# Kernel optimization log

Measured on AMD Instinct MI355X. Metric: run time of the kernel, lower is better.

## Reference

```python
import jax, jax.numpy as jnp
import numpy as np

# -------- configuration (production-scale segmentation head) --------
BS, C, H, W = 8, 256, 96, 96
N = H * W          # nodes in the spanning tree (flattened pixels)
E = N - 1          # spanning-tree edge count
ZETA_G = 0.01      # default zeta_g of Global_APro.forward


def setup_inputs() -> dict:
    key = jax.random.key(0)
    k1, k2 = jax.random.split(key)
    feature_in = jax.random.normal(k1, (BS, 1, H, W), dtype=jnp.float32)
    # scaled so norm2 distances over C=256 channels stay O(1..10)
    embed_in = 0.1 * jax.random.normal(k2, (BS, C, H, W), dtype=jnp.float32)
    # Random spanning trees, one per batch element. Edges are topologically
    # ordered: edge e connects parent=src[e] < child=tgt[e]=e+1, so processing
    # edges in order is a valid root->leaf sweep (and reversed is leaf->root).
    rng = np.random.default_rng(0)
    trees = []
    children = np.arange(1, N, dtype=np.int32)
    for _ in range(BS):
        parents = np.floor(rng.random(E) * np.arange(1, N)).astype(np.int32)
        trees.append(np.stack([parents, children], axis=1))
    tree = jnp.asarray(np.stack(trees, axis=0))  # [BS, E, 2] int32
    return {"feature_in": feature_in, "embed_in": embed_in, "tree": tree}


def _gp_single(f, wgt, src, tgt):
    """Global affinity propagation (tree filter) on one tree.
    Computes out_i = sum_j A_ij f_j / sum_j A_ij with A_ij = prod of edge
    affinities along the unique tree path i->j, via the classic two-pass DP.
    f: [N], wgt/src/tgt: [E] (edges topologically ordered, parent=src).
    """
    ones = jnp.ones_like(f)

    def up(carry, xs):                 # leaf -> root aggregation
        S, Z = carry
        s, t, we = xs
        S = S.at[s].add(we * S[t])
        Z = Z.at[s].add(we * Z[t])
        return (S, Z), None

    (S, Z), _ = jax.lax.scan(up, (f, ones), (src, tgt, wgt), reverse=True)

    def down(carry, xs):               # root -> leaf propagation
        F, G = carry
        s, t, we = xs
        F = F.at[t].set(we * F[s] + (1.0 - we * we) * F[t])
        G = G.at[t].set(we * G[s] + (1.0 - we * we) * G[t])
        return (F, G), None

    (F, G), _ = jax.lax.scan(down, (S, Z), (src, tgt, wgt))
    return F / G


def reference(feature_in, embed_in, tree):
    bs, c, h, w = embed_in.shape
    n = h * w
    emb = embed_in.reshape(bs, c, n)               # [bs, c, N]
    src = tree[:, :, 0]                            # [bs, E]
    tgt = tree[:, :, 1]                            # [bs, E]
    # gather node embeddings along tree edges (get_true_index)
    gather = jax.vmap(lambda e, i: e[:, i])        # [c, N], [E] -> [c, E]
    src_node = gather(emb, src)                    # [bs, c, E]
    tgt_node = gather(emb, tgt)                    # [bs, c, E]
    diff = src_node - tgt_node
    dist = jnp.sum(diff * diff, axis=1)            # norm2_distance -> [bs, E]
    wgt = jnp.exp(-ZETA_G * dist)                  # edge affinity
    f = feature_in.reshape(bs, n)                  # [bs, N]
    out = jax.vmap(_gp_single)(f, wgt, src, tgt)   # [bs, N]
    return out.reshape(bs, 1, h, w)
```

## Files before the change

### kernel.cpp

```cpp
#include <hip/hip_runtime.h>
#include <hip/hip_bf16.h>
#include <hip/hip_fp16.h>

#define BS 8
#define C  256
#define N  9216
#define E  9215
#define MAXD 128
#define LVL_STRIDE 192
#define NARROW 64
#define CPG 8
#define NG  (C / CPG)

typedef __attribute__((address_space(1))) const void GVoid;
typedef __attribute__((address_space(3))) void LVoid;

__global__ __launch_bounds__(1024) void setup_kernel(const float* __restrict__ emb,
                                                     const int* __restrict__ tree,
                                                     float* __restrict__ distG,
                                                     int* __restrict__ uparr,
                                                     int* __restrict__ lvlOff) {
    __shared__ int P[N];
    __shared__ int U[N];
    __shared__ int cnt8[MAXD * 8];
    __shared__ int tot[MAXD];
    __shared__ int sc1[MAXD];
    __shared__ int off[MAXD + 1];
    __shared__ int maxd_sh;
    const int tid = threadIdx.x;

    if (blockIdx.x >= BS) {
        const int wb = blockIdx.x - BS;
        const int b  = wb & 7;
        const int c0 = (wb >> 3) * CPG;
        const int wave = tid >> 6, lane = tid & 63;

        float* cur = (float*)P;
        float* nxt = (float*)U;

        int se[9];
        #pragma unroll
        for (int k = 0; k < 9; ++k) {
            int e = tid + k * 1024;
            se[k] = (e < E) ? tree[((size_t)b * E + e) * 2] : 0;
        }
        float acc[9];
        #pragma unroll
        for (int k = 0; k < 9; ++k) acc[k] = 0.f;

        const float* rowbase = emb + ((size_t)b * C + c0) * N;
        {
            const float* src = rowbase;
            for (int chk = wave; chk < 36; chk += 16)
                __builtin_amdgcn_global_load_lds(
                    (GVoid*)(src + chk * 256 + lane * 4),
                    (LVoid*)(cur + chk * 256), 16, 0, 0);
        }
        __syncthreads();

        for (int cc = 0; cc < CPG; ++cc) {
            if (cc + 1 < CPG) {
                const float* src = rowbase + (size_t)(cc + 1) * N;
                for (int chk = wave; chk < 36; chk += 16)
                    __builtin_amdgcn_global_load_lds(
                        (GVoid*)(src + chk * 256 + lane * 4),
                        (LVoid*)(nxt + chk * 256), 16, 0, 0);
            }
            #pragma unroll
            for (int k = 0; k < 9; ++k) {
                int e = tid + k * 1024;
                if (e < E) {
                    float d = cur[se[k]] - cur[e + 1];
                    acc[k] += d * d;
                }
            }
            __syncthreads();
            float* t = cur; cur = nxt; nxt = t;
        }
        #pragma unroll
        for (int k = 0; k < 9; ++k) {
            int e = tid + k * 1024;
            if (e < E) atomicAdd(&distG[(size_t)b * N + e], acc[k]);
        }
        return;
    }

    const int b = blockIdx.x;
    const int* tb = tree + b * E * 2;

    for (int t = tid; t < N; t += 1024)
        P[t] = (t == 0) ? 0 : (tb[(t - 1) * 2] | (1 << 16));
    for (int i = tid; i < MAXD * 8; i += 1024) cnt8[i] = 0;
    if (tid == 0) maxd_sh = 1;
    __syncthreads();

    for (int r = 0; r < 3; ++r) {
        for (int t = tid; t < N; t += 1024) {
            int p = P[t];
            int a = p & 0xffff;
            if (a == 0) U[t] = p;
            else {
                int pa = P[a];
                U[t] = (pa & 0xffff) | (((p >> 16) + (pa >> 16)) << 16);
            }
        }
        __syncthreads();
        for (int t = tid; t < N; t += 1024) {
            int p = U[t];
            int a = p & 0xffff;
            if (a == 0) P[t] = p;
            else {
                int pa = U[a];
                P[t] = (pa & 0xffff) | (((p >> 16) + (pa >> 16)) << 16);
            }
        }
        __syncthreads();
    }

    for (int t = 1 + tid; t < N; t += 1024) {
        int d = P[t] >> 16;
        atomicAdd(&cnt8[d * 8 + (tid >> 7)], 1);
    }
    __syncthreads();

    for (int d = tid; d < MAXD; d += 1024) {
        int s = 0;
        #pragma unroll
        for (int k = 0; k < 8; ++k) {
            int v = cnt8[d * 8 + k];
            cnt8[d * 8 + k] = s;
            s += v;
        }
        tot[d] = s;
        if (s > 0) atomicMax(&maxd_sh, d);
    }
    __syncthreads();

    {
        int* src = tot; int* dst = sc1;
        for (int step = 1; step < MAXD; step <<= 1) {
            for (int d = tid; d < MAXD; d += 1024)
                dst[d] = src[d] + ((d >= step) ? src[d - step] : 0);
            __syncthreads();
            int* tmp = src; src = dst; dst = tmp;
        }
        for (int d = tid; d < MAXD; d += 1024) off[d + 1] = src[d];
        if (tid == 0) off[0] = 0;
    }
    __syncthreads();

    if (tid == 0) {
        int md = maxd_sh;
        int lo = 0;
        while (lo < md && off[lo + 2] - off[lo + 1] <= NARROW) ++lo;
        int hi = md + 1;
        while (hi > lo + 1 && off[hi] - off[hi - 1] <= NARROW) --hi;
        lvlOff[b * LVL_STRIDE + 129] = md;
        lvlOff[b * LVL_STRIDE + 130] = lo;
        lvlOff[b * LVL_STRIDE + 131] = hi;
    }
    for (int t = 1 + tid; t < N; t += 1024) {
        int d = P[t] >> 16;
        int idx = atomicAdd(&cnt8[d * 8 + (tid >> 7)], 1);
        int slot = off[d] + idx;
        int p = tb[(t - 1) * 2];
        U[slot] = t | (p << 16);
    }
    __syncthreads();

    for (int i = tid; i < E; i += 1024) uparr[b * N + i] = U[i];
    for (int i = tid; i <= MAXD; i += 1024) lvlOff[b * LVL_STRIDE + i] = off[i];
}

__device__ __forceinline__ void up_edge(float2* V, const int2& ew) {
    int t = ew.x & 0xffff, p = ew.x >> 16;
    float w = __int_as_float(ew.y);
    float2 vt = V[t];
    atomicAdd(&V[p].x, w * vt.x);
    atomicAdd(&V[p].y, w * vt.y);
}

__device__ __forceinline__ void down_edge(float2* V, const int2& ew) {
    int t = ew.x & 0xffff, s = ew.x >> 16;
    float w = __int_as_float(ew.y);
    float2 vs = V[s], vt = V[t];
    float c = 1.f - w * w;
    V[t] = make_float2(w * vs.x + c * vt.x, w * vs.y + c * vt.y);
}

__global__ __launch_bounds__(512) void dp_kernel(const float* __restrict__ feat,
                                                 const int* __restrict__ lvlOff,
                                                 const int* __restrict__ uparr,
                                                 const float* __restrict__ distG,
                                                 float* __restrict__ out) {
    const int b = blockIdx.x;
    const int tid = threadIdx.x;
    __shared__ float2 V[N];
    __shared__ int2 TSW[N];
    __shared__ int off[MAXD + 1];
    __shared__ int meta[3];

    for (int i = tid; i <= MAXD; i += 512) off[i] = lvlOff[b * LVL_STRIDE + i];
    if (tid < 3) meta[tid] = lvlOff[b * LVL_STRIDE + 129 + tid];

    const int* uA = uparr + b * N;
    const float* dG = distG + b * N;
    for (int i = tid; i < N; i += 512)
        V[i] = make_float2(feat[b * N + i], 1.0f);
    for (int i = tid; i < E; i += 512) {
        int ts = uA[i];
        float ds = dG[(ts & 0xffff) - 1];
        TSW[i] = make_int2(ts, __float_as_int(__expf(-0.01f * ds)));
    }
    __syncthreads();
    const int maxd = meta[0], loE = meta[1], hiS = meta[2];

    if (tid < 64) {
        for (int lev = maxd; lev >= hiS; --lev) {
            int s0 = off[lev], s1 = off[lev + 1];
            for (int i = s0 + tid; i < s1; i += 64) up_edge(V, TSW[i]);
            __threadfence_block();
        }
    }
    __syncthreads();
    for (int lev = hiS - 1; lev > loE; --lev) {
        int s0 = off[lev], s1 = off[lev + 1];
        for (int i = s0 + tid; i < s1; i += 512) up_edge(V, TSW[i]);
        __syncthreads();
    }
    if (tid < 64) {
        for (int lev = loE; lev >= 1; --lev) {
            int s0 = off[lev], s1 = off[lev + 1];
            for (int i = s0 + tid; i < s1; i += 64) up_edge(V, TSW[i]);
            __threadfence_block();
        }
    }
    __syncthreads();

    if (tid < 64) {
        for (int lev = 1; lev <= loE; ++lev) {
            int s0 = off[lev], s1 = off[lev + 1];
            for (int i = s0 + tid; i < s1; i += 64) down_edge(V, TSW[i]);
            __threadfence_block();
        }
    }
    __syncthreads();
    for (int lev = loE + 1; lev < hiS; ++lev) {
        int s0 = off[lev], s1 = off[lev + 1];
        for (int i = s0 + tid; i < s1; i += 512) down_edge(V, TSW[i]);
        __syncthreads();
    }
    if (tid < 64) {
        for (int lev = hiS; lev <= maxd; ++lev) {
            int s0 = off[lev], s1 = off[lev + 1];
            for (int i = s0 + tid; i < s1; i += 64) down_edge(V, TSW[i]);
            __threadfence_block();
        }
    }
    __syncthreads();

    for (int i = tid; i < N; i += 512) {
        float2 v = V[i];
        out[b * N + i] = v.x / v.y;
    }
}

extern "C" void kernel_launch(void* const* d_in, const int* in_sizes, int n_in,
                              void* d_out, int out_size, void* d_ws, size_t ws_size,
                              hipStream_t stream) {
    const float* feat = (const float*)d_in[0];
    const float* emb  = (const float*)d_in[1];
    const int*   tree = (const int*)d_in[2];
    float* out = (float*)d_out;

    const size_t BN = (size_t)BS * N;
    float* distG  = (float*)d_ws;
    int*   uparr  = (int*)((char*)d_ws + BN * 4);
    int*   lvlOff = (int*)((char*)d_ws + BN * 8);

    hipMemsetAsync(distG, 0, BN * sizeof(float), stream);
    setup_kernel<<<BS + BS * NG, 1024, 0, stream>>>(emb, tree, distG, uparr, lvlOff);
    dp_kernel<<<BS, 512, 0, stream>>>(feat, lvlOff, uparr, distG, out);
}
```

Baseline: 167.9 us.

## Fuse setup and DP kernels via per-batch completion flags

Merges the level-sort/setup kernel and the tree DP kernel into one launch. The tree blocks keep their level-ordered edge lists in shared memory instead of writing them to global and reading them back. They then spin on a per-batch atomic counter until all distance blocks for that batch have finished accumulating. The channel group size is also doubled, which halves the number of distance blocks, and the DP now runs with 1024 threads. This removes a kernel launch boundary and a global round trip, but it relies on the distance blocks being co-resident or scheduled ahead of the spinning tree blocks. The DP blocks also need a larger shared-memory footprint.

New measurement: 214.8 us. +27.9%, slower.

```diff
diff --git a/kernel.cpp b/kernel.cpp
--- a/kernel.cpp
+++ b/kernel.cpp
@@ -7,25 +7,27 @@
 #define N  9216
 #define E  9215
 #define MAXD 128
-#define LVL_STRIDE 192
 #define NARROW 64
-#define CPG 8
+#define CPG 16
 #define NG  (C / CPG)
+#define NBLK (BS + BS * NG)
 
 typedef __attribute__((address_space(1))) const void GVoid;
 typedef __attribute__((address_space(3))) void LVoid;
 
-__global__ __launch_bounds__(1024) void setup_kernel(const float* __restrict__ emb,
+__global__ __launch_bounds__(1024) void fused_kernel(const float* __restrict__ feat,
+                                                     const float* __restrict__ emb,
                                                      const int* __restrict__ tree,
                                                      float* __restrict__ distG,
-                                                     int* __restrict__ uparr,
-                                                     int* __restrict__ lvlOff) {
-    __shared__ int P[N];
-    __shared__ int U[N];
+                                                     int* __restrict__ flagG,
+                                                     float* __restrict__ out) {
+    __shared__ float2 V[N];
+    __shared__ int2 TSW[N];
     __shared__ int cnt8[MAXD * 8];
     __shared__ int tot[MAXD];
     __shared__ int sc1[MAXD];
     __shared__ int off[MAXD + 1];
+    __shared__ int meta[3];
     __shared__ int maxd_sh;
     const int tid = threadIdx.x;
 
@@ -35,8 +37,8 @@
         const int c0 = (wb >> 3) * CPG;
         const int wave = tid >> 6, lane = tid & 63;
 
-        float* cur = (float*)P;
-        float* nxt = (float*)U;
+        float* cur = (float*)V;
+        float* nxt = (float*)V + N;
 
         int se[9];
         #pragma unroll
@@ -49,13 +51,10 @@
         for (int k = 0; k < 9; ++k) acc[k] = 0.f;
 
         const float* rowbase = emb + ((size_t)b * C + c0) * N;
-        {
-            const float* src = rowbase;
-            for (int chk = wave; chk < 36; chk += 16)
-                __builtin_amdgcn_global_load_lds(
-                    (GVoid*)(src + chk * 256 + lane * 4),
-                    (LVoid*)(cur + chk * 256), 16, 0, 0);
-        }
+        for (int chk = wave; chk < 36; chk += 16)
+            __builtin_amdgcn_global_load_lds(
+                (GVoid*)(rowbase + chk * 256 + lane * 4),
+                (LVoid*)(cur + chk * 256), 16, 0, 0);
         __syncthreads();
 
         for (int cc = 0; cc < CPG; ++cc) {
@@ -82,11 +81,18 @@
             int e = tid + k * 1024;
             if (e < E) atomicAdd(&distG[(size_t)b * N + e], acc[k]);
         }
+        __syncthreads();
+        __threadfence();
+        if (tid == 0)
+            __hip_atomic_fetch_add(&flagG[b], 1, __ATOMIC_RELEASE,
+                                   __HIP_MEMORY_SCOPE_AGENT);
         return;
     }
 
     const int b = blockIdx.x;
     const int* tb = tree + b * E * 2;
+    int* P = (int*)V;
+    int* U = ((int*)V) + N;
 
     for (int t = tid; t < N; t += 1024)
         P[t] = (t == 0) ? 0 : (tb[(t - 1) * 2] | (1 << 16));
@@ -155,62 +161,33 @@
         while (lo < md && off[lo + 2] - off[lo + 1] <= NARROW) ++lo;
         int hi = md + 1;
         while (hi > lo + 1 && off[hi] - off[hi - 1] <= NARROW) --hi;
-        lvlOff[b * LVL_STRIDE + 129] = md;
-        lvlOff[b * LVL_STRIDE + 130] = lo;
-        lvlOff[b * LVL_STRIDE + 131] = hi;
+        meta[0] = md; meta[1] = lo; meta[2] = hi;
     }
     for (int t = 1 + tid; t < N; t += 1024) {
         int d = P[t] >> 16;
         int idx = atomicAdd(&cnt8[d * 8 + (tid >> 7)], 1);
         int slot = off[d] + idx;
         int p = tb[(t - 1) * 2];
-        U[slot] = t | (p << 16);
-    }
-    __syncthreads();
-
-    for (int i = tid; i < E; i += 1024) uparr[b * N + i] = U[i];
-    for (int i = tid; i <= MAXD; i += 1024) lvlOff[b * LVL_STRIDE + i] = off[i];
-}
-
-__device__ __forceinline__ void up_edge(float2* V, const int2& ew) {
-    int t = ew.x & 0xffff, p = ew.x >> 16;
-    float w = __int_as_float(ew.y);
-    float2 vt = V[t];
-    atomicAdd(&V[p].x, w * vt.x);
-    atomicAdd(&V[p].y, w * vt.y);
-}
-
-__device__ __forceinline__ void down_edge(float2* V, const int2& ew) {
-    int t = ew.x & 0xffff, s = ew.x >> 16;
-    float w = __int_as_float(ew.y);
-    float2 vs = V[s], vt = V[t];
-    float c = 1.f - w * w;
-    V[t] = make_float2(w * vs.x + c * vt.x, w * vs.y + c * vt.y);
-}
-
-__global__ __launch_bounds__(512) void dp_kernel(const float* __restrict__ feat,
-                                                 const int* __restrict__ lvlOff,
-                                                 const int* __restrict__ uparr,
-                                                 const float* __restrict__ distG,
-                                                 float* __restrict__ out) {
-    const int b = blockIdx.x;
-    const int tid = threadIdx.x;
-    __shared__ float2 V[N];
-    __shared__ int2 TSW[N];
-    __shared__ int off[MAXD + 1];
-    __shared__ int meta[3];
-
-    for (int i = tid; i <= MAXD; i += 512) off[i] = lvlOff[b * LVL_STRIDE + i];
-    if (tid < 3) meta[tid] = lvlOff[b * LVL_STRIDE + 129 + tid];
-
-    const int* uA = uparr + b * N;
+        TSW[slot].x = t | (p << 16);
+    }
+    __syncthreads();
+
+    for (int i = tid; i < N; i += 1024)
+        V[i] = make_float2(feat[b * N + i], 1.0f);
+
+    if (tid == 0) {
+        while (__hip_atomic_load(&flagG[b], __ATOMIC_ACQUIRE,
+                                 __HIP_MEMORY_SCOPE_AGENT) < NG)
+            __builtin_amdgcn_s_sleep(8);
+    }
+    __syncthreads();
+
     const float* dG = distG + b * N;
-    for (int i = tid; i < N; i += 512)
-        V[i] = make_float2(feat[b * N + i], 1.0f);
-    for (int i = tid; i < E; i += 512) {
-        int ts = uA[i];
-        float ds = dG[(ts & 0xffff) - 1];
-        TSW[i] = make_int2(ts, __float_as_int(__expf(-0.01f * ds)));
+    for (int i = tid; i < E; i += 1024) {
+        int ts = TSW[i].x;
+        float ds = __hip_atomic_load(&dG[(ts & 0xffff) - 1], __ATOMIC_RELAXED,
+                                     __HIP_MEMORY_SCOPE_AGENT);
+        TSW[i].y = __float_as_int(__expf(-0.01f * ds));
     }
     __syncthreads();
     const int maxd = meta[0], loE = meta[1], hiS = meta[2];
@@ -218,20 +195,41 @@
     if (tid < 64) {
         for (int lev = maxd; lev >= hiS; --lev) {
             int s0 = off[lev], s1 = off[lev + 1];
-            for (int i = s0 + tid; i < s1; i += 64) up_edge(V, TSW[i]);
+            for (int i = s0 + tid; i < s1; i += 64) {
+                int2 ew = TSW[i];
+                int t = ew.x & 0xffff, p = ew.x >> 16;
+                float w = __int_as_float(ew.y);
+                float2 vt = V[t];
+                atomicAdd(&V[p].x, w * vt.x);
+                atomicAdd(&V[p].y, w * vt.y);
+            }
             __threadfence_block();
         }
     }
     __syncthreads();
     for (int lev = hiS - 1; lev > loE; --lev) {
         int s0 = off[lev], s1 = off[lev + 1];
-        for (int i = s0 + tid; i < s1; i += 512) up_edge(V, TSW[i]);
+        for (int i = s0 + tid; i < s1; i += 1024) {
+            int2 ew = TSW[i];
+            int t = ew.x & 0xffff, p = ew.x >> 16;
+            float w = __int_as_float(ew.y);
+            float2 vt = V[t];
+            atomicAdd(&V[p].x, w * vt.x);
+            atomicAdd(&V[p].y, w * vt.y);
+        }
         __syncthreads();
     }
     if (tid < 64) {
         for (int lev = loE; lev >= 1; --lev) {
             int s0 = off[lev], s1 = off[lev + 1];
-            for (int i = s0 + tid; i < s1; i += 64) up_edge(V, TSW[i]);
+            for (int i = s0 + tid; i < s1; i += 64) {
+                int2 ew = TSW[i];
+                int t = ew.x & 0xffff, p = ew.x >> 16;
+                float w = __int_as_float(ew.y);
+                float2 vt = V[t];
+                atomicAdd(&V[p].x, w * vt.x);
+                atomicAdd(&V[p].y, w * vt.y);
+            }
             __threadfence_block();
         }
     }
@@ -240,26 +238,47 @@
     if (tid < 64) {
         for (int lev = 1; lev <= loE; ++lev) {
             int s0 = off[lev], s1 = off[lev + 1];
-            for (int i = s0 + tid; i < s1; i += 64) down_edge(V, TSW[i]);
+            for (int i = s0 + tid; i < s1; i += 64) {
+                int2 ew = TSW[i];
+                int t = ew.x & 0xffff, s = ew.x >> 16;
+                float w = __int_as_float(ew.y);
+                float2 vs = V[s], vt = V[t];
+                float c = 1.f - w * w;
+                V[t] = make_float2(w * vs.x + c * vt.x, w * vs.y + c * vt.y);
+            }
             __threadfence_block();
         }
     }
     __syncthreads();
     for (int lev = loE + 1; lev < hiS; ++lev) {
         int s0 = off[lev], s1 = off[lev + 1];
-        for (int i = s0 + tid; i < s1; i += 512) down_edge(V, TSW[i]);
+        for (int i = s0 + tid; i < s1; i += 1024) {
+            int2 ew = TSW[i];
+            int t = ew.x & 0xffff, s = ew.x >> 16;
+            float w = __int_as_float(ew.y);
+            float2 vs = V[s], vt = V[t];
+            float c = 1.f - w * w;
+            V[t] = make_float2(w * vs.x + c * vt.x, w * vs.y + c * vt.y);
+        }
         __syncthreads();
     }
     if (tid < 64) {
         for (int lev = hiS; lev <= maxd; ++lev) {
             int s0 = off[lev], s1 = off[lev + 1];
-            for (int i = s0 + tid; i < s1; i += 64) down_edge(V, TSW[i]);
+            for (int i = s0 + tid; i < s1; i += 64) {
+                int2 ew = TSW[i];
+                int t = ew.x & 0xffff, s = ew.x >> 16;
+                float w = __int_as_float(ew.y);
+                float2 vs = V[s], vt = V[t];
+                float c = 1.f - w * w;
+                V[t] = make_float2(w * vs.x + c * vt.x, w * vs.y + c * vt.y);
+            }
             __threadfence_block();
         }
     }
     __syncthreads();
 
-    for (int i = tid; i < N; i += 512) {
+    for (int i = tid; i < N; i += 1024) {
         float2 v = V[i];
         out[b * N + i] = v.x / v.y;
     }
@@ -274,11 +293,9 @@
     float* out = (float*)d_out;
 
     const size_t BN = (size_t)BS * N;
-    float* distG  = (float*)d_ws;
-    int*   uparr  = (int*)((char*)d_ws + BN * 4);
-    int*   lvlOff = (int*)((char*)d_ws + BN * 8);
-
-    hipMemsetAsync(distG, 0, BN * sizeof(float), stream);
-    setup_kernel<<<BS + BS * NG, 1024, 0, stream>>>(emb, tree, distG, uparr, lvlOff);
-    dp_kernel<<<BS, 512, 0, stream>>>(feat, lvlOff, uparr, distG, out);
+    float* distG = (float*)d_ws;
+    int*   flagG = (int*)((char*)d_ws + BN * 4);
+
+    hipMemsetAsync(d_ws, 0, BN * 4 + 256, stream);
+    fused_kernel<<<NBLK, 1024, 0, stream>>>(feat, emb, tree, distG, flagG, out);
 }
```
